# Kernel tuning notes

Hardware: AMD Instinct MI355X
Metric: run time of the kernel (lower is better)

The kernel has to match this reference:

```python
import jax, jax.numpy as jnp
import numpy as np

HEADS = 8
DIM_HEAD = 64
NUM_MEM_KV = 4

def rmsnorm(x, g):
    # F.normalize(x, dim=1) * g * sqrt(C): L2-normalize over channel dim with eps clamp
    n = jnp.sqrt(jnp.sum(x * x, axis=1, keepdims=True))
    return x / jnp.maximum(n, 1e-12) * g * (x.shape[1] ** 0.5)

def setup_inputs() -> dict:
    key = jax.random.key(0)
    ks = jax.random.split(key, 7)
    b, c, h, w = 32, 512, 32, 32
    hidden = HEADS * DIM_HEAD
    x = jax.random.normal(ks[0], (b, c, h, w), jnp.float32)
    g_in = 1.0 + 0.02 * jax.random.normal(ks[1], (1, c, 1, 1), jnp.float32)
    w_qkv = jax.random.normal(ks[2], (3 * hidden, c), jnp.float32) * (c ** -0.5)
    mem_kv = jax.random.normal(ks[3], (2, HEADS, DIM_HEAD, NUM_MEM_KV), jnp.float32)
    w_out = jax.random.normal(ks[4], (c, hidden), jnp.float32) * (hidden ** -0.5)
    b_out = 0.01 * jax.random.normal(ks[5], (c,), jnp.float32)
    g_out = 1.0 + 0.02 * jax.random.normal(ks[6], (1, c, 1, 1), jnp.float32)
    return {"x": x, "g_in": g_in, "w_qkv": w_qkv, "mem_kv": mem_kv,
            "w_out": w_out, "b_out": b_out, "g_out": g_out}

def reference(x, g_in, w_qkv, mem_kv, w_out, b_out, g_out):
    b, c, h, w = x.shape
    scale = DIM_HEAD ** -0.5
    xn = rmsnorm(x, g_in)
    # 1x1 conv (no bias) == channel GEMM
    qkv = jnp.einsum('bchw,oc->bohw', xn, w_qkv)
    q, k, v = jnp.split(qkv, 3, axis=1)
    to_heads = lambda t: t.reshape(b, HEADS, DIM_HEAD, h * w)  # b (h c) x y -> b h c (xy)
    q, k, v = map(to_heads, (q, k, v))
    mk = jnp.broadcast_to(mem_kv[0], (b,) + mem_kv[0].shape)
    mv = jnp.broadcast_to(mem_kv[1], (b,) + mem_kv[1].shape)
    k = jnp.concatenate([mk, k], axis=-1)
    v = jnp.concatenate([mv, v], axis=-1)
    q = jax.nn.softmax(q, axis=-2) * scale   # softmax over feature dim d
    k = jax.nn.softmax(k, axis=-1)           # softmax over sequence dim n
    context = jnp.einsum('bhdn,bhen->bhde', k, v)
    out = jnp.einsum('bhde,bhdn->bhen', context, q)
    out = out.reshape(b, HEADS * DIM_HEAD, h, w)
    out = jnp.einsum('bchw,oc->bohw', out, w_out) + b_out[None, :, None, None]
    return rmsnorm(out, g_out)
```

## Files before the change

kernel.cpp:

```cpp
#include <hip/hip_runtime.h>
#include <hip/hip_bf16.h>


#define AS1 __attribute__((address_space(1)))
#define AS3 __attribute__((address_space(3)))

using short8 = __attribute__((ext_vector_type(8))) short;
using usht4  = __attribute__((ext_vector_type(4))) unsigned short;
using f32x4  = __attribute__((ext_vector_type(4))) float;

__device__ __forceinline__ unsigned short f2bf(float f) {
  unsigned int u = __float_as_uint(f);
  u += 0x7fffu + ((u >> 16) & 1u);
  return (unsigned short)(u >> 16);
}
__device__ __forceinline__ float bf2f(unsigned short s) {
  return __uint_as_float(((unsigned int)s) << 16);
}

__global__ __launch_bounds__(256, 4)
void norm_r(const float* __restrict__ X, float* __restrict__ R) {
  __shared__ float part[32][33];
  const int t = threadIdx.x;
  const int b = blockIdx.x >> 5;
  const int pos0 = (blockIdx.x & 31) * 32;
  const int pg = t & 7, cg = t >> 3;
  const float* xp = X + ((size_t)b * 512 + (size_t)cg * 16) * 1024 + pos0 + pg * 4;
  f32x4 s = {0.f, 0.f, 0.f, 0.f};
#pragma unroll
  for (int i = 0; i < 16; ++i) {
    f32x4 v = *(const f32x4*)(xp + (size_t)i * 1024);
    s += v * v;
  }
  part[cg][pg * 4 + 0] = s.x;
  part[cg][pg * 4 + 1] = s.y;
  part[cg][pg * 4 + 2] = s.z;
  part[cg][pg * 4 + 3] = s.w;
  __syncthreads();
  if (t < 32) {
    float tot = 0.f;
#pragma unroll
    for (int j = 0; j < 32; ++j) tot += part[j][t];
    R[(size_t)b * 1024 + pos0 + t] = 22.627416998f / fmaxf(sqrtf(tot), 1e-12f);
  }
}

__global__ __launch_bounds__(256, 4)
void norm_r_bf16(const unsigned short* __restrict__ X, float* __restrict__ R) {
  __shared__ float part[16][64];
  const int t = threadIdx.x;
  const int b = blockIdx.x >> 4;
  const int pos0 = (blockIdx.x & 15) * 64;
  const int pg = t & 15, cg = t >> 4;
  const unsigned short* xp =
      X + ((size_t)b * 512 + (size_t)cg * 32) * 1024 + pos0 + pg * 4;
  float s0 = 0.f, s1 = 0.f, s2 = 0.f, s3 = 0.f;
#pragma unroll 8
  for (int i = 0; i < 32; ++i) {
    usht4 v = *(const usht4*)(xp + (size_t)i * 1024);
    float a = bf2f(v.x), bb = bf2f(v.y), c = bf2f(v.z), d = bf2f(v.w);
    s0 += a * a; s1 += bb * bb; s2 += c * c; s3 += d * d;
  }
  part[cg][pg * 4 + 0] = s0;
  part[cg][pg * 4 + 1] = s1;
  part[cg][pg * 4 + 2] = s2;
  part[cg][pg * 4 + 3] = s3;
  __syncthreads();
  if (t < 64) {
    float tot = 0.f;
#pragma unroll
    for (int j = 0; j < 16; ++j) tot += part[j][t];
    R[(size_t)b * 1024 + pos0 + t] = 22.627416998f / fmaxf(sqrtf(tot), 1e-12f);
  }
}

__global__ __launch_bounds__(256, 4)
void xn_transpose(const float* __restrict__ X, const float* __restrict__ R,
                  unsigned short* __restrict__ XT) {
  __shared__ float tile[64][65];
  const int t = threadIdx.x;
  const int b = blockIdx.z, cb = blockIdx.y, pb = blockIdx.x;
  {
    const int p = t & 63, cg = t >> 6;
    const float r = R[(size_t)b * 1024 + pb * 64 + p];
    const float* xp = X + ((size_t)b * 512 + (size_t)(cb * 64 + cg * 16)) * 1024 + pb * 64 + p;
#pragma unroll
    for (int i = 0; i < 16; ++i)
      tile[cg * 16 + i][p] = xp[(size_t)i * 1024] * r;
  }
  __syncthreads();
#pragma unroll
  for (int k = 0; k < 2; ++k) {
    const int idx = k * 256 + t;
    const int p = idx >> 3, c8 = idx & 7;
    short8 v;
#pragma unroll
    for (int j = 0; j < 8; ++j) v[j] = (short)f2bf(tile[c8 * 8 + j][p]);
    *(short8*)(XT + ((size_t)b * 1024 + pb * 64 + p) * 512 + cb * 64 + c8 * 8) = v;
  }
}

__global__ __launch_bounds__(256, 4)
void cast_wqkv(const float* __restrict__ W, const float* __restrict__ g,
               unsigned short* __restrict__ O) {
  int i = blockIdx.x * 256 + threadIdx.x;
  O[i] = f2bf(W[i] * g[i & 511]);
}
__global__ __launch_bounds__(256, 4)
void cast_w(const float* __restrict__ W, unsigned short* __restrict__ O, int n) {
  int i = blockIdx.x * 256 + threadIdx.x;
  if (i < n) O[i] = f2bf(W[i]);
}

template <int MTOT, bool SPLIT3, bool BIAS>
__global__ __launch_bounds__(512, 2)
void gemm_bt(const unsigned short* __restrict__ A,
             const unsigned short* __restrict__ Ball,
             unsigned short* __restrict__ O0, unsigned short* __restrict__ O1,
             unsigned short* __restrict__ O2, const float* __restrict__ bias) {
  __shared__ __align__(16) unsigned short smem[65536];
  const int t = threadIdx.x;
  const int lane = t & 63, w = t >> 6;
  const int wm = w >> 2, wn = w & 3;
  const int mt = blockIdx.x >> 2, nt = blockIdx.x & 3;
  const int b = blockIdx.y;
  const unsigned short* Ag = A + (size_t)(mt * 256) * 512;
  const unsigned short* Bg = Ball + ((size_t)b * 1024 + (size_t)nt * 256) * 512;

  const int r0 = t >> 2;
  const int csrc = (t & 3) ^ ((r0 >> 1) & 3);
  const unsigned short* As0 = Ag + (size_t)r0 * 512 + csrc * 8;
  const unsigned short* Bs0 = Bg + (size_t)r0 * 512 + csrc * 8;

  auto STAGE = [&](int kt) {
    unsigned short* dst = smem + (kt & 3) * 16384 + w * 512;
    const size_t ko = (size_t)kt * 32;
#pragma unroll
    for (int i = 0; i < 2; ++i) {
      __builtin_amdgcn_global_load_lds(
          (const AS1 unsigned int*)(As0 + ko + (size_t)i * 65536),
          (AS3 unsigned int*)(dst + i * 4096), 16, 0, 0);
      __builtin_amdgcn_global_load_lds(
          (const AS1 unsigned int*)(Bs0 + ko + (size_t)i * 65536),
          (AS3 unsigned int*)(dst + 8192 + i * 4096), 16, 0, 0);
    }
  };

  f32x4 acc[8][4] = {};
  const int fsw = (((lane >> 4) ^ ((lane >> 1) & 3)) << 3);
  const int am = (lane & 15);

  STAGE(0); STAGE(1); STAGE(2);
#pragma unroll 1
  for (int kt = 0; kt < 16; ++kt) {
    asm volatile("s_waitcnt vmcnt(8)" ::: "memory");
    __builtin_amdgcn_s_barrier();
    asm volatile("" ::: "memory");
    const unsigned short* lA = smem + (kt & 3) * 16384;
    const unsigned short* lB = lA + 8192;
    short8 af[8], bf[4];
#pragma unroll
    for (int i = 0; i < 8; ++i) {
      const int row = wm * 128 + i * 16 + am;
      af[i] = *(const short8*)(lA + row * 32 + fsw);
    }
#pragma unroll
    for (int j = 0; j < 4; ++j) {
      const int row = wn * 64 + j * 16 + am;
      bf[j] = *(const short8*)(lB + row * 32 + fsw);
    }
    STAGE((kt + 3) & 15);
    __builtin_amdgcn_s_setprio(1);
#pragma unroll
    for (int i = 0; i < 8; ++i)
#pragma unroll
      for (int j = 0; j < 4; ++j)
        acc[i][j] = __builtin_amdgcn_mfma_f32_16x16x32_bf16(af[i], bf[j],
                                                            acc[i][j], 0, 0, 0);
    __builtin_amdgcn_s_setprio(0);
  }

  asm volatile("s_waitcnt vmcnt(0)" ::: "memory");
  __syncthreads();
  unsigned short* Cw = smem + w * 8192;
#pragma unroll
  for (int i = 0; i < 8; ++i)
#pragma unroll
    for (int j = 0; j < 4; ++j)
#pragma unroll
      for (int r = 0; r < 4; ++r) {
        const int row = i * 16 + (lane >> 4) * 4 + r;
        const int col = j * 16 + (lane & 15);
        float v = acc[i][j][r];
        if (BIAS) v += bias[mt * 256 + wm * 128 + row];
        Cw[row * 64 + col] = f2bf(v);
      }
  unsigned short* Og;
  if (SPLIT3) {
    const int sec = mt >> 1;
    unsigned short* base = (sec == 0) ? O0 : ((sec == 1) ? O1 : O2);
    Og = base + ((size_t)b * 512 + (size_t)((mt & 1) * 256 + wm * 128)) * 1024 +
         nt * 256 + wn * 64;
  } else {
    Og = O0 + ((size_t)b * MTOT + (size_t)(mt * 256 + wm * 128)) * 1024 +
         nt * 256 + wn * 64;
  }
#pragma unroll
  for (int p = 0; p < 16; ++p) {
    const int row = p * 8 + (lane >> 3);
    short8 v = *(const short8*)(Cw + row * 64 + (lane & 7) * 8);
    *(short8*)(Og + (size_t)row * 1024 + (lane & 7) * 8) = v;
  }
}

__global__ __launch_bounds__(256, 2)
void attn_kernel(const unsigned short* __restrict__ Qp,
                 const unsigned short* __restrict__ Kp,
                 const unsigned short* __restrict__ Vp,
                 const float* __restrict__ memkv,
                 unsigned short* __restrict__ outT) {
  __shared__ char smem[36608];
  unsigned short* bufA = (unsigned short*)smem;
  unsigned short* bufB = (unsigned short*)(smem + 9216);
  float* Pl   = (float*)(smem + 18432);
  float* Pc   = (float*)(smem + 18432);
  float* csS  = (float*)(smem + 21504);
  float* msum = (float*)(smem + 35072);
  float* rsI  = (float*)(smem + 36096);
  const int t = threadIdx.x;
  const int lane = t & 63, wave = t >> 6;
  const int b = blockIdx.x >> 3, h = blockIdx.x & 7;
  const size_t hb = ((size_t)b * 512 + (size_t)h * 64) * 1024;
  const unsigned short* Qg = Qp + hb;
  const unsigned short* Kg = Kp + hb;
  const unsigned short* Vg = Vp + hb;
  const float* mk = memkv + (size_t)h * 256;
  const float* mv = memkv + 2048 + (size_t)h * 256;

  float rsum[2] = {0.f, 0.f};
  f32x4 cacc[4] = {};

  for (int it = 0; it < 17; ++it) {
    if (it == 0) {
      const int d = t & 63, j = t >> 6;
      const float ev = __expf(mk[d * 4 + j]);
      msum[d * 4 + j] = ev;
      bufA[d * 72 + j] = f2bf(ev);
      bufB[d * 72 + j] = f2bf(mv[d * 4 + j]);
      for (int c2 = 4 + j; c2 < 64; c2 += 4) {
        bufA[d * 72 + c2] = 0;
        bufB[d * 72 + c2] = 0;
      }
    } else {
      const int c0 = (it - 1) * 64;
#pragma unroll
      for (int z = 0; z < 2; ++z) {
        const int d = z * 32 + (t >> 3), ch = t & 7;
        short8 kv = *(const short8*)(Kg + (size_t)d * 1024 + c0 + ch * 8);
        short8 pk;
        float ssum = 0.f;
#pragma unroll
        for (int j = 0; j < 8; ++j) {
          const float e = __expf(bf2f((unsigned short)kv[j]));
          ssum += e;
          pk[j] = (short)f2bf(e);
        }
        rsum[z] += ssum;
        *(short8*)(bufA + d * 72 + ch * 8) = pk;
        short8 vv = *(const short8*)(Vg + (size_t)d * 1024 + c0 + ch * 8);
        *(short8*)(bufB + d * 72 + ch * 8) = vv;
      }
    }
    __syncthreads();
#pragma unroll
    for (int ks = 0; ks < 2; ++ks) {
      short8 a = *(const short8*)(bufA + (wave * 16 + (lane & 15)) * 72 +
                                  ks * 32 + (lane >> 4) * 8);
#pragma unroll
      for (int et = 0; et < 4; ++et) {
        short8 bb = *(const short8*)(bufB + (et * 16 + (lane & 15)) * 72 +
                                     ks * 32 + (lane >> 4) * 8);
        cacc[et] = __builtin_amdgcn_mfma_f32_16x16x32_bf16(a, bb, cacc[et], 0, 0, 0);
      }
    }
    __syncthreads();
  }

  Pl[t]       = rsum[0];
  Pl[256 + t] = rsum[1];
  __syncthreads();
  if (t < 64) {
    float s = 0.f;
#pragma unroll
    for (int ch = 0; ch < 8; ++ch) s += Pl[t * 8 + ch];
    s += msum[t * 4] + msum[t * 4 + 1] + msum[t * 4 + 2] + msum[t * 4 + 3];
    rsI[t] = 1.0f / s;
  }
  __syncthreads();

  unsigned short* CT = bufB;
#pragma unroll
  for (int et = 0; et < 4; ++et)
#pragma unroll
    for (int r = 0; r < 4; ++r) {
      const int d = wave * 16 + (lane >> 4) * 4 + r;
      const int e = et * 16 + (lane & 15);
      CT[e * 72 + d] = f2bf(cacc[et][r] * rsI[d]);
    }
  __syncthreads();

  short8 a0 = *(const short8*)(CT + (wave * 16 + (lane & 15)) * 72 + (lane >> 4) * 8);
  short8 a1 = *(const short8*)(CT + (wave * 16 + (lane & 15)) * 72 + 32 + (lane >> 4) * 8);
  unsigned short* oBase = outT + (size_t)b * 1024 * 512 + h * 64;

  for (int pt = 0; pt < 16; ++pt) {
    {
      const int p = lane, dq = wave;
      float cp = 0.f;
#pragma unroll
      for (int i2 = 0; i2 < 8; ++i2) {
        const int d0 = dq * 16 + i2 * 2;
        const float e0 = __expf(bf2f(Qg[(size_t)d0 * 1024 + pt * 64 + p]));
        const float e1 = __expf(bf2f(Qg[(size_t)(d0 + 1) * 1024 + pt * 64 + p]));
        cp += e0 + e1;
        const unsigned int pk =
            (unsigned int)f2bf(e0) | ((unsigned int)f2bf(e1) << 16);
        *(unsigned int*)(bufA + p * 72 + d0) = pk;
      }
      Pc[dq * 64 + p] = cp;
    }
    __syncthreads();
    if (t < 64) csS[t] = 0.125f / (Pc[t] + Pc[64 + t] + Pc[128 + t] + Pc[192 + t]);
    __syncthreads();
#pragma unroll
    for (int ps = 0; ps < 4; ++ps) {
      f32x4 oc = {};
      short8 b0 = *(const short8*)(bufA + (ps * 16 + (lane & 15)) * 72 + (lane >> 4) * 8);
      short8 b1 = *(const short8*)(bufA + (ps * 16 + (lane & 15)) * 72 + 32 + (lane >> 4) * 8);
      oc = __builtin_amdgcn_mfma_f32_16x16x32_bf16(a0, b0, oc, 0, 0, 0);
      oc = __builtin_amdgcn_mfma_f32_16x16x32_bf16(a1, b1, oc, 0, 0, 0);
      const float cs = csS[ps * 16 + (lane & 15)];
      const unsigned long long pk =
          (unsigned long long)f2bf(oc[0] * cs) |
          ((unsigned long long)f2bf(oc[1] * cs) << 16) |
          ((unsigned long long)f2bf(oc[2] * cs) << 32) |
          ((unsigned long long)f2bf(oc[3] * cs) << 48);
      const int p = pt * 64 + ps * 16 + (lane & 15);
      *(unsigned long long*)(oBase + (size_t)p * 512 + wave * 16 + (lane >> 4) * 4) = pk;
    }
    __syncthreads();
  }
}

__global__ __launch_bounds__(256, 4)
void final_scale_bf16(const unsigned short* __restrict__ P,
                      const float* __restrict__ R, const float* __restrict__ G,
                      float* __restrict__ O) {
  const size_t f = ((size_t)blockIdx.x * 256 + threadIdx.x) * 4;
  const int p = (int)(f & 1023);
  const int c = (int)((f >> 10) & 511);
  const int b = (int)(f >> 19);
  usht4 v = *(const usht4*)(P + f);
  const f32x4 r = *(const f32x4*)(R + (size_t)b * 1024 + p);
  const float g = G[c];
  f32x4 o;
  o.x = bf2f(v.x) * r.x * g;
  o.y = bf2f(v.y) * r.y * g;
  o.z = bf2f(v.z) * r.z * g;
  o.w = bf2f(v.w) * r.w * g;
  *(f32x4*)(O + f) = o;
}

extern "C" void kernel_launch(void* const* d_in, const int* in_sizes, int n_in,
                              void* d_out, int out_size, void* d_ws, size_t ws_size,
                              hipStream_t stream) {
  (void)in_sizes; (void)n_in; (void)out_size; (void)ws_size;
  const float* x     = (const float*)d_in[0];
  const float* g_in  = (const float*)d_in[1];
  const float* w_qkv = (const float*)d_in[2];
  const float* memkv = (const float*)d_in[3];
  const float* w_out = (const float*)d_in[4];
  const float* b_out = (const float*)d_in[5];
  const float* g_out = (const float*)d_in[6];
  float* out = (float*)d_out;

  char* ws = (char*)d_ws;
  float* r1           = (float*)ws;
  float* r2           = (float*)(ws + 131072);
  unsigned short* wqb = (unsigned short*)(ws + 262144);
  unsigned short* wob = (unsigned short*)(ws + 1835008);
  unsigned short* xnT = (unsigned short*)(ws + 2359296);
  unsigned short* Qp  = (unsigned short*)(ws + 35913728);
  unsigned short* outT = xnT;
  unsigned short* pre  = Qp;
  unsigned short* Kp  = (unsigned short*)d_out;
  unsigned short* Vp  = (unsigned short*)d_out + 16777216;

  norm_r<<<1024, 256, 0, stream>>>(x, r1);
  xn_transpose<<<dim3(16, 8, 32), 256, 0, stream>>>(x, r1, xnT);
  cast_wqkv<<<3072, 256, 0, stream>>>(w_qkv, g_in, wqb);
  cast_w<<<1024, 256, 0, stream>>>(w_out, wob, 262144);
  gemm_bt<1536, true, false><<<dim3(24, 32), 512, 0, stream>>>(
      wqb, xnT, Qp, Kp, Vp, nullptr);
  attn_kernel<<<256, 256, 0, stream>>>(Qp, Kp, Vp, memkv, outT);
  gemm_bt<512, false, true><<<dim3(8, 32), 512, 0, stream>>>(
      wob, outT, pre, nullptr, nullptr, b_out);
  norm_r_bf16<<<512, 256, 0, stream>>>(pre, r2);
  final_scale_bf16<<<16384, 256, 0, stream>>>(pre, r2, g_out, out);
}
```

Before: 273.4 us.

## Restructure GEMM main loop into interleaved half-tile load/MFMA phases with swizzled epilogue

The bf16 GEMM main loop now uses 64-wide K tiles with double buffering. Each tile is split into four phases that alternate issuing one global-to-LDS stage with 16 MFMAs, separated by barriers, replacing the former 4-deep ring of 32-wide K stages. The epilogue write of C into LDS uses an XOR swizzle on column blocks to cut bank conflicts, and the readback un-swizzles it. The aim is to hide load latency behind the MFMAs and to lower LDS conflicts. The cost is more barriers per iteration and a shallower prefetch distance.

```diff
diff --git a/kernel.cpp b/kernel.cpp
--- a/kernel.cpp
+++ b/kernel.cpp
@@ -127,90 +127,144 @@
   const unsigned short* Ag = A + (size_t)(mt * 256) * 512;
   const unsigned short* Bg = Ball + ((size_t)b * 1024 + (size_t)nt * 256) * 512;
 
-  const int r0 = t >> 2;
-  const int csrc = (t & 3) ^ ((r0 >> 1) & 3);
-  const unsigned short* As0 = Ag + (size_t)r0 * 512 + csrc * 8;
-  const unsigned short* Bs0 = Bg + (size_t)r0 * 512 + csrc * 8;
-
-  auto STAGE = [&](int kt) {
-    unsigned short* dst = smem + (kt & 3) * 16384 + w * 512;
-    const size_t ko = (size_t)kt * 32;
-#pragma unroll
-    for (int i = 0; i < 2; ++i) {
+  const int srow = w * 16 + (lane >> 2);
+  const int schunk8 = ((lane & 3) ^ ((lane >> 3) & 3)) * 8;
+  const int fr = lane & 15;
+  const int slotoff = (((lane >> 4) ^ ((lane >> 1) & 3)) << 3);
+  const int aBase = (wm * 128 + fr) * 32 + slotoff;
+  const int bBase = (wn * 64 + fr) * 32 + slotoff;
+
+  f32x4 acc[8][4] = {};
+
+  auto STAGE = [&](int kt, int kh, int isB) {
+    const unsigned short* Xg = isB ? Bg : Ag;
+    unsigned short* plane = smem + (kt & 1) * 32768 + isB * 16384 + kh * 8192;
+    const size_t kofs = (size_t)((kt & 7) * 64 + kh * 32 + schunk8);
+#pragma unroll
+    for (int j = 0; j < 2; ++j)
       __builtin_amdgcn_global_load_lds(
-          (const AS1 unsigned int*)(As0 + ko + (size_t)i * 65536),
-          (AS3 unsigned int*)(dst + i * 4096), 16, 0, 0);
-      __builtin_amdgcn_global_load_lds(
-          (const AS1 unsigned int*)(Bs0 + ko + (size_t)i * 65536),
-          (AS3 unsigned int*)(dst + 8192 + i * 4096), 16, 0, 0);
-    }
+          (const AS1 unsigned int*)(Xg + (size_t)(j * 128 + srow) * 512 + kofs),
+          (AS3 unsigned int*)(plane + (j * 128 + w * 16) * 32), 16, 0, 0);
   };
 
-  f32x4 acc[8][4] = {};
-  const int fsw = (((lane >> 4) ^ ((lane >> 1) & 3)) << 3);
-  const int am = (lane & 15);
-
-  STAGE(0); STAGE(1); STAGE(2);
+#define GBAR() asm volatile("" ::: "memory"); \
+               __builtin_amdgcn_s_barrier();  \
+               asm volatile("" ::: "memory")
+#define MFMA_BF16 __builtin_amdgcn_mfma_f32_16x16x32_bf16
+
+  STAGE(0, 0, 0); STAGE(0, 0, 1); STAGE(0, 1, 0); STAGE(0, 1, 1);
+  asm volatile("s_waitcnt vmcnt(4)" ::: "memory");
+  GBAR();
+
 #pragma unroll 1
-  for (int kt = 0; kt < 16; ++kt) {
-    asm volatile("s_waitcnt vmcnt(8)" ::: "memory");
-    __builtin_amdgcn_s_barrier();
-    asm volatile("" ::: "memory");
-    const unsigned short* lA = smem + (kt & 3) * 16384;
-    const unsigned short* lB = lA + 8192;
-    short8 af[8], bf[4];
+  for (int kt = 0; kt < 8; ++kt) {
+    const unsigned short* lAp = smem + (kt & 1) * 32768;
+    const unsigned short* lBp = lAp + 16384;
+    const int ktn = kt + 1;
+    short8 af[8], bf0, bf1;
+
+#pragma unroll
+    for (int i = 0; i < 8; ++i)
+      af[i] = *(const short8*)(lAp + aBase + i * 512);
+    bf0 = *(const short8*)(lBp + bBase);
+    bf1 = *(const short8*)(lBp + bBase + 512);
+    STAGE(ktn, 0, 0);
+    GBAR();
+    __builtin_amdgcn_sched_barrier(0);
+    __builtin_amdgcn_s_setprio(1);
 #pragma unroll
     for (int i = 0; i < 8; ++i) {
-      const int row = wm * 128 + i * 16 + am;
-      af[i] = *(const short8*)(lA + row * 32 + fsw);
-    }
+      acc[i][0] = MFMA_BF16(af[i], bf0, acc[i][0], 0, 0, 0);
+      acc[i][1] = MFMA_BF16(af[i], bf1, acc[i][1], 0, 0, 0);
+    }
+    __builtin_amdgcn_s_setprio(0);
+    GBAR();
+
+    bf0 = *(const short8*)(lBp + bBase + 1024);
+    bf1 = *(const short8*)(lBp + bBase + 1536);
+    STAGE(ktn, 0, 1);
+    asm volatile("s_waitcnt vmcnt(4)" ::: "memory");
+    GBAR();
+    __builtin_amdgcn_sched_barrier(0);
+    __builtin_amdgcn_s_setprio(1);
+#pragma unroll
+    for (int i = 0; i < 8; ++i) {
+      acc[i][2] = MFMA_BF16(af[i], bf0, acc[i][2], 0, 0, 0);
+      acc[i][3] = MFMA_BF16(af[i], bf1, acc[i][3], 0, 0, 0);
+    }
+    __builtin_amdgcn_s_setprio(0);
+    GBAR();
+
+#pragma unroll
+    for (int i = 0; i < 8; ++i)
+      af[i] = *(const short8*)(lAp + 8192 + aBase + i * 512);
+    bf0 = *(const short8*)(lBp + 8192 + bBase);
+    bf1 = *(const short8*)(lBp + 8192 + bBase + 512);
+    STAGE(ktn, 1, 0);
+    GBAR();
+    __builtin_amdgcn_sched_barrier(0);
+    __builtin_amdgcn_s_setprio(1);
+#pragma unroll
+    for (int i = 0; i < 8; ++i) {
+      acc[i][0] = MFMA_BF16(af[i], bf0, acc[i][0], 0, 0, 0);
+      acc[i][1] = MFMA_BF16(af[i], bf1, acc[i][1], 0, 0, 0);
+    }
+    __builtin_amdgcn_s_setprio(0);
+    GBAR();
+
+    bf0 = *(const short8*)(lBp + 8192 + bBase + 1024);
+    bf1 = *(const short8*)(lBp + 8192 + bBase + 1536);
+    STAGE(ktn, 1, 1);
+    asm volatile("s_waitcnt vmcnt(4)" ::: "memory");
+    GBAR();
+    __builtin_amdgcn_sched_barrier(0);
+    __builtin_amdgcn_s_setprio(1);
+#pragma unroll
+    for (int i = 0; i < 8; ++i) {
+      acc[i][2] = MFMA_BF16(af[i], bf0, acc[i][2], 0, 0, 0);
+      acc[i][3] = MFMA_BF16(af[i], bf1, acc[i][3], 0, 0, 0);
+    }
+    __builtin_amdgcn_s_setprio(0);
+    GBAR();
+  }
+
+  asm volatile("s_waitcnt vmcnt(0)" ::: "memory");
+  __syncthreads();
+  unsigned short* Cw = smem + w * 8192;
+  const int g = lane >> 4, l15 = lane & 15;
+#pragma unroll
+  for (int i = 0; i < 8; ++i)
 #pragma unroll
     for (int j = 0; j < 4; ++j) {
-      const int row = wn * 64 + j * 16 + am;
-      bf[j] = *(const short8*)(lB + row * 32 + fsw);
-    }
-    STAGE((kt + 3) & 15);
-    __builtin_amdgcn_s_setprio(1);
-#pragma unroll
-    for (int i = 0; i < 8; ++i)
-#pragma unroll
-      for (int j = 0; j < 4; ++j)
-        acc[i][j] = __builtin_amdgcn_mfma_f32_16x16x32_bf16(af[i], bf[j],
-                                                            acc[i][j], 0, 0, 0);
-    __builtin_amdgcn_s_setprio(0);
-  }
-
-  asm volatile("s_waitcnt vmcnt(0)" ::: "memory");
-  __syncthreads();
-  unsigned short* Cw = smem + w * 8192;
-#pragma unroll
-  for (int i = 0; i < 8; ++i)
-#pragma unroll
-    for (int j = 0; j < 4; ++j)
+      const int cs = ((j ^ g) << 4) + l15;
 #pragma unroll
       for (int r = 0; r < 4; ++r) {
-        const int row = i * 16 + (lane >> 4) * 4 + r;
-        const int col = j * 16 + (lane & 15);
+        const int row = i * 16 + g * 4 + r;
         float v = acc[i][j][r];
         if (BIAS) v += bias[mt * 256 + wm * 128 + row];
-        Cw[row * 64 + col] = f2bf(v);
+        Cw[row * 64 + cs] = f2bf(v);
       }
-  unsigned short* Og;
+    }
+  unsigned short* OgW;
   if (SPLIT3) {
     const int sec = mt >> 1;
     unsigned short* base = (sec == 0) ? O0 : ((sec == 1) ? O1 : O2);
-    Og = base + ((size_t)b * 512 + (size_t)((mt & 1) * 256 + wm * 128)) * 1024 +
-         nt * 256 + wn * 64;
+    OgW = base + ((size_t)b * 512 + (size_t)((mt & 1) * 256 + wm * 128)) * 1024 +
+          nt * 256 + wn * 64;
   } else {
-    Og = O0 + ((size_t)b * MTOT + (size_t)(mt * 256 + wm * 128)) * 1024 +
-         nt * 256 + wn * 64;
+    OgW = O0 + ((size_t)b * MTOT + (size_t)(mt * 256 + wm * 128)) * 1024 +
+          nt * 256 + wn * 64;
   }
 #pragma unroll
   for (int p = 0; p < 16; ++p) {
     const int row = p * 8 + (lane >> 3);
-    short8 v = *(const short8*)(Cw + row * 64 + (lane & 7) * 8);
-    *(short8*)(Og + (size_t)row * 1024 + (lane & 7) * 8) = v;
-  }
+    const int q2 = (row >> 2) & 3;
+    const int slot = (lane & 7) ^ (q2 << 1);
+    short8 v = *(const short8*)(Cw + row * 64 + slot * 8);
+    *(short8*)(OgW + (size_t)row * 1024 + (lane & 7) * 8) = v;
+  }
+#undef GBAR
+#undef MFMA_BF16
 }
 
 __global__ __launch_bounds__(256, 2)
```

Measured after the change: 282.6 us. 3.4% more time.
